# Kernel optimization log

Hardware: AMD Instinct MI355X
Metric: run time of the kernel (lower is better)

Reference implementation:

```python
import jax, jax.numpy as jnp
import numpy as np

SEQ_LEN = 768
PRED_LEN = 192
ENC_IN = 321
BATCH = 2
N_ORDER = 256
MULTISCALE = (1, 2, 4)
MODES = 32  # min(32, min(pred_len, seq_len)//2)


def _transition(N):
    Q = np.arange(N, dtype=np.float64)
    R = (2 * Q + 1)[:, None]
    j, i = np.meshgrid(Q, Q)
    A = np.where(i < j, -1, (-1.0) ** (i - j + 1)) * R
    B = (-1.0) ** Q[:, None] * R
    return A, B


def _hippo_legt(N, dt):
    # bilinear (Tustin) discretization, identical to scipy.signal.cont2discrete(..., method='bilinear')
    A, Bc = _transition(N)
    I = np.eye(N)
    M = I - (dt / 2.0) * A
    Ad = np.linalg.solve(M, I + (dt / 2.0) * A)
    Bd = np.linalg.solve(M, dt * Bc)[:, 0]
    # eval_matrix: Legendre P_n(1 - 2*vals), vals = arange(0, 1, dt)
    vals = np.arange(0.0, 1.0, dt)
    x = 1.0 - 2.0 * vals
    P = np.zeros((len(vals), N))
    P[:, 0] = 1.0
    if N > 1:
        P[:, 1] = x
    for n in range(1, N - 1):
        P[:, n + 1] = ((2 * n + 1) * x * P[:, n] - n * P[:, n - 1]) / (n + 1)
    return Ad.astype(np.float32), Bd.astype(np.float32), P.astype(np.float32)


def setup_inputs() -> dict:
    key = jax.random.key(0)
    k = jax.random.split(key, 6)
    A_l, B_l, E_l = [], [], []
    for ms in MULTISCALE:
        Ad, Bd, E = _hippo_legt(N_ORDER, 1.0 / PRED_LEN / ms)
        A_l.append(Ad); B_l.append(Bd); E_l.append(jnp.asarray(E))
    scale = 1.0 / (N_ORDER * N_ORDER)
    return {
        "history_data": jax.random.normal(k[0], (BATCH, SEQ_LEN, ENC_IN, 1), jnp.float32),
        "future_data": jax.random.normal(k[1], (BATCH, PRED_LEN, ENC_IN, 1), jnp.float32),
        "affine_weight": jnp.ones((1, 1, ENC_IN), jnp.float32),
        "affine_bias": jnp.zeros((1, 1, ENC_IN), jnp.float32),
        "A_stack": jnp.asarray(np.stack(A_l)),            # [3, N, N]
        "B_stack": jnp.asarray(np.stack(B_l)),            # [3, N]
        "E0": E_l[0], "E1": E_l[1], "E2": E_l[2],        # [ms*pred, N]
        "wr": scale * jax.random.uniform(k[2], (3, N_ORDER, N_ORDER, MODES), jnp.float32),
        "wi": scale * jax.random.uniform(k[3], (3, N_ORDER, N_ORDER, MODES), jnp.float32),
        "mlp_w": 0.3 * jax.random.normal(k[4], (1, 3), jnp.float32),
        "mlp_b": jnp.zeros((1,), jnp.float32),
        "batch_seen": 0, "epoch": 1, "train": 1,
    }


def _hippo_scan(x_in, A, Bv):
    # x_in: [B, Lw, H] -> states [Lw, B, H, N]
    inp = jnp.transpose(x_in, (1, 0, 2))  # [Lw, B, H]
    c0 = jnp.zeros(x_in.shape[:1] + x_in.shape[2:] + (A.shape[0],), x_in.dtype)  # [B, H, N]
    def step(c, f):
        c = c @ A.T + f[..., None] * Bv
        return c, c
    _, cs = jax.lax.scan(step, c0, inp)
    return cs


def _forward(history_data, affine_weight, affine_bias, A_stack, B_stack, evals, wr, wi, mlp_w, mlp_b):
    x_enc = history_data[:, :, :, 0]                      # [B, L, H]
    means = jax.lax.stop_gradient(jnp.mean(x_enc, axis=1, keepdims=True))
    x = x_enc - means
    stdev = jax.lax.stop_gradient(jnp.sqrt(jnp.mean(x * x, axis=1, keepdims=True) + 1e-5))
    x = x / stdev * affine_weight + affine_bias

    x_decs = []
    for i, ms in enumerate(MULTISCALE):
        Lw = ms * PRED_LEN
        x_in = x[:, -Lw:]                                  # [B, Lw, H]
        cs = _hippo_scan(x_in, A_stack[i], B_stack[i])     # [Lw, B, H, N]
        xc = jnp.transpose(cs, (1, 2, 3, 0))               # [B, H, N, Lw]
        # spectral conv: rfft -> complex mode mixing over N -> irfft
        xf = jnp.fft.rfft(xc)                              # [B, H, N, Lw//2+1]
        a = xf[..., :MODES]
        W = wr[i] + 1j * wi[i]                             # [N, N, MODES]
        of = jnp.einsum('bjix,iox->bjox', a, W)
        out_ft = jnp.pad(of, ((0, 0), (0, 0), (0, 0), (0, Lw // 2 + 1 - MODES)))
        o = jnp.fft.irfft(out_ft, n=Lw)                    # [B, H, N, Lw]
        x_dec_c = o[:, :, :, PRED_LEN - 1]                 # [B, H, N]
        x_dec = x_dec_c @ evals[i][-PRED_LEN:].T           # [B, H, pred]
        x_decs.append(x_dec)

    xd = jnp.stack(x_decs, axis=-1)                        # [B, H, pred, 3]
    xd = jnp.einsum('bhpk,k->bhp', xd, mlp_w[0]) + mlp_b[0]
    xd = jnp.transpose(xd, (0, 2, 1))                      # [B, pred, H]
    xd = (xd - affine_bias) / (affine_weight + 1e-10)
    xd = xd * stdev + means
    return xd[..., None]                                   # [B, pred, H, 1]


def reference(history_data, future_data, affine_weight, affine_bias, A_stack, B_stack, E0, E1, E2, wr, wi, mlp_w, mlp_b, batch_seen, epoch, train):
    return _forward(history_data, affine_weight, affine_bias, A_stack, B_stack, (E0, E1, E2), wr, wi, mlp_w, mlp_b)
```

## Files before the change

### kernel.cpp

```cpp
#include <hip/hip_runtime.h>

#define SEQ 768
#define PRED 192
#define ENC 321
#define NB 2
#define BE (NB*ENC)
#define CH 32

typedef float vf2 __attribute__((ext_vector_type(2)));
typedef short s4v __attribute__((ext_vector_type(4)));
typedef short s8v __attribute__((ext_vector_type(8)));
typedef float f32x4 __attribute__((ext_vector_type(4)));

union F4V2 { float4 f4; vf2 v2[2]; };
union S8U { s4v h[2]; s8v v; };

__device__ __forceinline__ float4 ldg4(const float* p) {
    return *reinterpret_cast<const float4*>(p);
}
__device__ __forceinline__ s8v ldg8s(const unsigned short* p) {
    return *reinterpret_cast<const s8v*>(p);
}
__device__ __forceinline__ void pklo(vf2& c, vf2 a, vf2 b) {
    asm("v_pk_fma_f32 %0, %1, %2, %0 op_sel:[0,0,0] op_sel_hi:[0,1,1]"
        : "+v"(c) : "v"(a), "v"(b));
}
__device__ __forceinline__ void pkhi(vf2& c, vf2 a, vf2 b) {
    asm("v_pk_fma_f32 %0, %1, %2, %0 op_sel:[1,0,0] op_sel_hi:[1,1,1]"
        : "+v"(c) : "v"(a), "v"(b));
}

__device__ __forceinline__ unsigned short f2bf(float f) {
    unsigned int u = __float_as_uint(f);
    u = (u + 0x7fffu + ((u >> 16) & 1u)) >> 16;
    return (unsigned short)u;
}
__device__ __forceinline__ float bf2f(unsigned short h) {
    return __uint_as_float(((unsigned int)h) << 16);
}

__host__ __device__ __forceinline__ int d_Lw(int s)    { return s==0?192:(s==1?384:768); }
__host__ __device__ __forceinline__ int d_Hoff(int s)  { return s==0?0:(s==1?49152:147456); }
__host__ __device__ __forceinline__ int d_twoff(int s) { return s==0?0:(s==1?6144:18432); }
__host__ __device__ __forceinline__ int d_Coff(int s)  { return s==0?0:(s==1?3145728:9437184); }
__host__ __device__ __forceinline__ int d_rowoff(int s){ return s==0?0:(s==1?192:576); }

__global__ void __launch_bounds__(256) k_init0(
    float2* __restrict__ twm, float2* __restrict__ gtm,
    const float* __restrict__ Ast, const float* __restrict__ Bst,
    float* __restrict__ apow, float* __restrict__ Hbuf,
    const float* __restrict__ hist, float* __restrict__ ps, float* __restrict__ ps2,
    const float* __restrict__ wr, const float* __restrict__ wi,
    unsigned short* __restrict__ Bph, unsigned short* __restrict__ Bpl)
{
    __shared__ float smem[128*36];
    int bid = blockIdx.x;
    int t = threadIdx.x;
    if (bid < 168) {
        int i = bid*256 + t;
        if (i >= 43008) return;
        int s, rem;
        if (i < 6144)       { s=0; rem=i; }
        else if (i < 18432) { s=1; rem=i-6144; }
        else                { s=2; rem=i-18432; }
        int Lw = d_Lw(s);
        int k = rem & 31, m = rem >> 5;
        const float TWO_PI = 6.28318530717958647692f;
        int km = (k*m) % Lw;
        float c, sn;
        sincosf(TWO_PI * km / Lw, &sn, &c);
        twm[i] = make_float2(c, -sn);
        int e = (k*(PRED-1-m)) % Lw; if (e < 0) e += Lw;
        float c2, s2v;
        sincosf(TWO_PI * e / Lw, &s2v, &c2);
        float coef = (k==0 ? 1.f : 2.f) / (float)Lw;
        gtm[i] = make_float2(coef*c2, coef*s2v);
    } else if (bid < 936) {
        int i = (bid-168)*256 + t;
        if (i < 3*65536) apow[i] = Ast[i];
        if (i < 3*256) {
            int s = i >> 8, n = i & 255;
            Hbuf[d_Hoff(s) + n] = Bst[i];
        }
    } else if (bid < 1032) {
        int r = bid - 936;
        int bx = r % 6, b = (r/6) % 2, z = r / 12;
        int jx = t & 63, ty = t >> 6;
        int j = bx*64 + jx;
        float s = 0.f, s2 = 0.f;
        if (j < ENC) {
            int t0 = z*96;
            for (int tt = t0 + ty; tt < t0 + 96; tt += 4) {
                float v = hist[(size_t)b*SEQ*ENC + (size_t)tt*ENC + j];
                s += v; s2 += v*v;
            }
        }
        float* l1 = smem;
        float* l2 = smem + 256;
        l1[ty*64+jx] = s; l2[ty*64+jx] = s2;
        __syncthreads();
        if (ty == 0 && j < ENC) {
            float S  = l1[jx]+l1[64+jx]+l1[128+jx]+l1[192+jx];
            float S2 = l2[jx]+l2[64+jx]+l2[128+jx]+l2[192+jx];
            ps [((size_t)z*2 + b)*ENC + j] = S;
            ps2[((size_t)z*2 + b)*ENC + j] = S2;
        }
    } else {
        int r = bid - 1032;
        int o  = r & 255;
        int q0 = ((r >> 8) & 1) * 128;
        int s  = r >> 9;
        const float* wrS = wr + (size_t)s*2097152;
        const float* wiS = wi + (size_t)s*2097152;
        unsigned short* BphS = Bph + (size_t)s*4194304;
        unsigned short* BplS = Bpl + (size_t)s*4194304;
        float (*ldsq)[36] = reinterpret_cast<float(*)[36]>(smem);
        int qr = t >> 1, half = (t & 1)*16;
        int kk = t & 31, qc = t >> 5;
        for (int c = 0; c < 2; c++) {
            const float* W = (c ? wiS : wrS) + (size_t)(q0+qr)*8192 + o*32 + half;
            float4 v0 = ldg4(W), v1 = ldg4(W+4), v2 = ldg4(W+8), v3 = ldg4(W+12);
            __syncthreads();
            *reinterpret_cast<float4*>(&ldsq[qr][half+0])  = v0;
            *reinterpret_cast<float4*>(&ldsq[qr][half+4])  = v1;
            *reinterpret_cast<float4*>(&ldsq[qr][half+8])  = v2;
            *reinterpret_cast<float4*>(&ldsq[qr][half+12]) = v3;
            __syncthreads();
            unsigned short hbuf[16], lbuf[16];
            #pragma unroll
            for (int j = 0; j < 16; j++) {
                float f = ldsq[qc*16 + j][kk];
                unsigned short h = f2bf(f);
                hbuf[j] = h;
                lbuf[j] = f2bf(f - bf2f(h));
            }
            int col = o*64 + kk*2 + c;
            int qb  = q0 + qc*16;
            size_t off = (size_t)(qb >> 5)*524288 + (size_t)col*32 + (qb & 31);
            #pragma unroll
            for (int j = 0; j < 2; j++) {
                *reinterpret_cast<s8v*>(BphS + off + j*8) = *reinterpret_cast<s8v*>(&hbuf[j*8]);
                *reinterpret_cast<s8v*>(BplS + off + j*8) = *reinterpret_cast<s8v*>(&lbuf[j*8]);
            }
        }
    }
}

__global__ void k_stats2(const float* __restrict__ ps, const float* __restrict__ ps2,
                         float* __restrict__ meanb, float* __restrict__ stdb) {
    int i = blockIdx.x*256 + threadIdx.x;
    if (i >= BE) return;
    int b = i / ENC, j = i - b*ENC;
    float S = 0.f, S2 = 0.f;
    #pragma unroll
    for (int z = 0; z < 8; z++) {
        S  += ps [((size_t)z*2 + b)*ENC + j];
        S2 += ps2[((size_t)z*2 + b)*ENC + j];
    }
    float m   = S * (1.f/SEQ);
    float var = S2 * (1.f/SEQ) - m*m;
    meanb[b*ENC+j] = m;
    stdb[b*ENC+j]  = sqrtf(var + 1e-5f);
}

__global__ void k_norm(const float* __restrict__ hist,
                       const float* __restrict__ meanb, const float* __restrict__ stdb,
                       const float* __restrict__ aw, const float* __restrict__ ab,
                       float* __restrict__ xn) {
    int i = blockIdx.x*256 + threadIdx.x;
    if (i >= NB*SEQ*ENC) return;
    int j = i % ENC;
    int b = i / (SEQ*ENC);
    float v = (hist[i] - meanb[b*ENC+j]) / stdb[b*ENC+j];
    xn[i] = v * aw[j] + ab[j];
}

__device__ __forceinline__ void gemm32nt(float* As, float* Bs,
    const float* __restrict__ A, int Arows, const float* __restrict__ B,
    float* __restrict__ C, int m0, int n0)
{
    int tid = threadIdx.x;
    int tm = tid >> 4, tn = tid & 15;
    int lr = tid >> 3, lq = (tid & 7)*4;
    float a00=0.f,a01=0.f,a10=0.f,a11=0.f;
    for (int kt = 0; kt < 256; kt += 32) {
        __syncthreads();
        float4 fa = ldg4(A + (size_t)(m0+lr)*256 + kt + lq);
        float4 fb = ldg4(B + (size_t)(n0+lr)*256 + kt + lq);
        As[lr*33+lq]=fa.x; As[lr*33+lq+1]=fa.y; As[lr*33+lq+2]=fa.z; As[lr*33+lq+3]=fa.w;
        Bs[lr*33+lq]=fb.x; Bs[lr*33+lq+1]=fb.y; Bs[lr*33+lq+2]=fb.z; Bs[lr*33+lq+3]=fb.w;
        __syncthreads();
        #pragma unroll
        for (int q = 0; q < 32; q++) {
            float x0 = As[(tm*2)*33+q],  x1 = As[(tm*2+1)*33+q];
            float y0 = Bs[(tn*2)*33+q],  y1 = Bs[(tn*2+1)*33+q];
            a00 = fmaf(x0,y0,a00); a01 = fmaf(x0,y1,a01);
            a10 = fmaf(x1,y0,a10); a11 = fmaf(x1,y1,a11);
        }
    }
    int m = m0 + tm*2, n = n0 + tn*2;
    if (m < Arows)   { C[(size_t)m*256+n]     = a00; C[(size_t)m*256+n+1]     = a01; }
    if (m+1 < Arows) { C[(size_t)(m+1)*256+n] = a10; C[(size_t)(m+1)*256+n+1] = a11; }
}

__device__ __forceinline__ void gemm32nn(float* As, float* Bs,
    const float* __restrict__ A, const float* __restrict__ B,
    float* __restrict__ C, int m0, int n0)
{
    int tid = threadIdx.x;
    int tm = tid >> 4, tn = tid & 15;
    int lr = tid >> 3, lq = (tid & 7)*4;
    float a00=0.f,a01=0.f,a10=0.f,a11=0.f;
    for (int kt = 0; kt < 256; kt += 32) {
        __syncthreads();
        float4 fa = ldg4(A + (size_t)(m0+lr)*256 + kt + lq);
        float4 fb = ldg4(B + (size_t)(kt+lr)*256 + n0 + lq);
        As[lr*33+lq]=fa.x; As[lr*33+lq+1]=fa.y; As[lr*33+lq+2]=fa.z; As[lr*33+lq+3]=fa.w;
        Bs[lr*33+lq]=fb.x; Bs[lr*33+lq+1]=fb.y; Bs[lr*33+lq+2]=fb.z; Bs[lr*33+lq+3]=fb.w;
        __syncthreads();
        #pragma unroll
        for (int q = 0; q < 32; q++) {
            float x0 = As[(tm*2)*33+q], x1 = As[(tm*2+1)*33+q];
            float y0 = Bs[q*33+tn*2],   y1 = Bs[q*33+tn*2+1];
            a00 = fmaf(x0,y0,a00); a01 = fmaf(x0,y1,a01);
            a10 = fmaf(x1,y0,a10); a11 = fmaf(x1,y1,a11);
        }
    }
    int m = m0 + tm*2, n = n0 + tn*2;
    C[(size_t)m*256+n]     = a00; C[(size_t)m*256+n+1]     = a01;
    C[(size_t)(m+1)*256+n] = a10; C[(size_t)(m+1)*256+n+1] = a11;
}

__global__ void __launch_bounds__(256) k_hlevel32(float* __restrict__ Hbuf,
                                                  float* __restrict__ apow,
                                                  int par, int mc) {
    __shared__ float As[32*33];
    __shared__ float Bs[32*33];
    int s = blockIdx.z;
    int Lw = d_Lw(s);
    const float* Asrc = apow + (size_t)par*196608 + (size_t)s*65536;
    float* Adst       = apow + (size_t)(1-par)*196608 + (size_t)s*65536;
    float* H = Hbuf + d_Hoff(s);
    int yt = blockIdx.y, xt = blockIdx.x;
    if (yt < 8) {
        if (mc >= Lw) return;
        int rows = min(mc, Lw - mc);
        if (yt*32 >= rows) return;
        gemm32nt(As, Bs, H, rows, Asrc, H + (size_t)mc*256, yt*32, xt*32);
    } else {
        if (2*mc >= Lw) return;
        gemm32nn(As, Bs, Asrc, Asrc, Adst, (yt-8)*32, xt*32);
    }
}

__global__ void k_split_h(const float* __restrict__ Hbuf,
                          unsigned short* __restrict__ Hh,
                          unsigned short* __restrict__ Hl) {
    int i = blockIdx.x*256 + threadIdx.x;
    if (i >= 344064) return;
    int s, rem;
    if (i < 49152)       { s=0; rem=i; }
    else if (i < 147456) { s=1; rem=i-49152; }
    else                 { s=2; rem=i-147456; }
    int Lw = d_Lw(s);
    int row = rem >> 8, q = rem & 255;
    float f = Hbuf[i];
    unsigned short h = f2bf(f);
    float l = f - bf2f(h);
    size_t off = (size_t)d_Hoff(s) + (size_t)(q >> 5)*((size_t)Lw*32) + (size_t)row*32 + (q & 31);
    Hh[off] = h;
    Hl[off] = f2bf(l);
}

__device__ __forceinline__ s8v lds_frag(const short* s, int idx) {
    S8U u;
    u.h[0] = *reinterpret_cast<const s4v*>(s + idx);
    u.h[1] = *reinterpret_cast<const s4v*>(s + idx + 4);
    return u.v;
}

__global__ void __launch_bounds__(256) k_cgemm_mfma(
    const unsigned short* __restrict__ Hh, const unsigned short* __restrict__ Hl,
    const unsigned short* __restrict__ Bph, const unsigned short* __restrict__ Bpl,
    float* __restrict__ C)
{
    int t = threadIdx.x;
    int nwg = gridDim.x;
    int cpx = nwg >> 3;
    int bid = blockIdx.x;
    int lid = (bid & 7)*cpx + (bid >> 3);
    int s, local, mt;
    if (lid < 256)      { s = 0; local = lid;       mt = 2; }
    else if (lid < 640) { s = 1; local = lid - 256; mt = 3; }
    else                { s = 2; local = lid - 640; mt = 6; }
    int Lw = d_Lw(s);
    int bx = local % mt, by = local / mt;
    int m0 = bx*128, n0 = by*128;

    const unsigned short* HhS = Hh + d_Hoff(s);
    const unsigned short* HlS = Hl + d_Hoff(s);
    const unsigned short* BphS = Bph + (size_t)s*4194304;
    const unsigned short* BplS = Bpl + (size_t)s*4194304;
    float* CS = C + d_Coff(s);

    __shared__ short sA[2][128*36];
    __shared__ short sB[2][128*36];
    int lane = t & 63, wave = t >> 6;
    int wm = wave >> 1, wn = wave & 1;
    int srow = t >> 1, shalf = (t & 1)*16;
    size_t strideA = (size_t)Lw*32;
    size_t aRow = (size_t)(m0 + srow)*32 + shalf;
    size_t bRow = (size_t)(n0 + srow)*32 + shalf;
    int sOff = srow*36 + shalf;

    f32x4 acc[4][4];
    #pragma unroll
    for (int i = 0; i < 4; i++)
        #pragma unroll
        for (int j = 0; j < 4; j++)
            acc[i][j] = (f32x4){0.f, 0.f, 0.f, 0.f};

    S8U ah0, ah1, al0, al1, bh0, bh1, bl0, bl1;
    ah0.v = ldg8s(HhS + aRow);
    ah1.v = ldg8s(HhS + aRow + 8);
    al0.v = ldg8s(HlS + aRow);
    al1.v = ldg8s(HlS + aRow + 8);
    bh0.v = ldg8s(BphS + bRow);
    bh1.v = ldg8s(BphS + bRow + 8);
    bl0.v = ldg8s(BplS + bRow);
    bl1.v = ldg8s(BplS + bRow + 8);

    for (int kt = 0; kt < 256; kt += 32) {
        __syncthreads();
        *reinterpret_cast<s4v*>(&sA[0][sOff+0])  = ah0.h[0];
        *reinterpret_cast<s4v*>(&sA[0][sOff+4])  = ah0.h[1];
        *reinterpret_cast<s4v*>(&sA[0][sOff+8])  = ah1.h[0];
        *reinterpret_cast<s4v*>(&sA[0][sOff+12]) = ah1.h[1];
        *reinterpret_cast<s4v*>(&sA[1][sOff+0])  = al0.h[0];
        *reinterpret_cast<s4v*>(&sA[1][sOff+4])  = al0.h[1];
        *reinterpret_cast<s4v*>(&sA[1][sOff+8])  = al1.h[0];
        *reinterpret_cast<s4v*>(&sA[1][sOff+12]) = al1.h[1];
        *reinterpret_cast<s4v*>(&sB[0][sOff+0])  = bh0.h[0];
        *reinterpret_cast<s4v*>(&sB[0][sOff+4])  = bh0.h[1];
        *reinterpret_cast<s4v*>(&sB[0][sOff+8])  = bh1.h[0];
        *reinterpret_cast<s4v*>(&sB[0][sOff+12]) = bh1.h[1];
        *reinterpret_cast<s4v*>(&sB[1][sOff+0])  = bl0.h[0];
        *reinterpret_cast<s4v*>(&sB[1][sOff+4])  = bl0.h[1];
        *reinterpret_cast<s4v*>(&sB[1][sOff+8])  = bl1.h[0];
        *reinterpret_cast<s4v*>(&sB[1][sOff+12]) = bl1.h[1];
        __syncthreads();
        if (kt + 32 < 256) {
            int kb = (kt >> 5) + 1;
            ah0.v = ldg8s(HhS + kb*strideA + aRow);
            ah1.v = ldg8s(HhS + kb*strideA + aRow + 8);
            al0.v = ldg8s(HlS + kb*strideA + aRow);
            al1.v = ldg8s(HlS + kb*strideA + aRow + 8);
            bh0.v = ldg8s(BphS + (size_t)kb*524288 + bRow);
            bh1.v = ldg8s(BphS + (size_t)kb*524288 + bRow + 8);
            bl0.v = ldg8s(BplS + (size_t)kb*524288 + bRow);
            bl1.v = ldg8s(BplS + (size_t)kb*524288 + bRow + 8);
        }
        int klane = (lane >> 4) << 3;
        s8v Bfh[4], Bfl[4];
        #pragma unroll
        for (int tn = 0; tn < 4; tn++) {
            int cb = (wn*64 + tn*16 + (lane & 15))*36 + klane;
            Bfh[tn] = lds_frag(sB[0], cb);
            Bfl[tn] = lds_frag(sB[1], cb);
        }
        #pragma unroll
        for (int tm = 0; tm < 4; tm++) {
            int ca = (wm*64 + tm*16 + (lane & 15))*36 + klane;
            s8v Ah = lds_frag(sA[0], ca);
            s8v Al = lds_frag(sA[1], ca);
            #pragma unroll
            for (int tn = 0; tn < 4; tn++) {
                acc[tm][tn] = __builtin_amdgcn_mfma_f32_16x16x32_bf16(Ah, Bfh[tn], acc[tm][tn], 0, 0, 0);
                acc[tm][tn] = __builtin_amdgcn_mfma_f32_16x16x32_bf16(Ah, Bfl[tn], acc[tm][tn], 0, 0, 0);
                acc[tm][tn] = __builtin_amdgcn_mfma_f32_16x16x32_bf16(Al, Bfh[tn], acc[tm][tn], 0, 0, 0);
            }
        }
    }
    int r0 = (lane >> 4)*4, cc = lane & 15;
    #pragma unroll
    for (int tm = 0; tm < 4; tm++) {
        #pragma unroll
        for (int tn = 0; tn < 4; tn++) {
            int gcol = n0 + wn*64 + tn*16 + cc;
            int og = gcol >> 6, rem = gcol & 63;
            float* cp = CS + (size_t)og*((size_t)Lw*64) + rem;
            #pragma unroll
            for (int reg = 0; reg < 4; reg++) {
                int r = m0 + wm*64 + tm*16 + r0 + reg;
                if (r < Lw) cp[(size_t)r*64] = acc[tm][tn][reg];
            }
        }
    }
}

__global__ void k_cscan1(const float2* __restrict__ Call2, const float2* __restrict__ twm,
                         float2* __restrict__ psum) {
    int cg = blockIdx.x;
    int s  = (cg < 6) ? 0 : (cg < 18) ? 1 : 2;
    int cl = cg - ((s==0)?0:(s==1)?6:18);
    int Lw = d_Lw(s);
    int tid = threadIdx.x;
    int k = tid & 31, ol = tid >> 5;
    int o = blockIdx.y*8 + ol;
    const float2* tws = twm + d_twoff(s);
    const float2* Co = Call2 + (d_Coff(s) >> 1) + (size_t)o*((size_t)Lw*32);
    int mbase = cl*CH;
    float pr = 0.f, pi = 0.f;
    for (int mm = 0; mm < CH; mm++) {
        int m = mbase + mm;
        float2 cc = Co[(size_t)m*32 + k];
        float2 t  = tws[(size_t)m*32 + k];
        pr = fmaf(t.x, cc.x, pr); pr = fmaf(-t.y, cc.y, pr);
        pi = fmaf(t.x, cc.y, pi); pi = fmaf(t.y, cc.x, pi);
    }
    psum[((size_t)cg)*8192 + o*32 + k] = make_float2(pr, pi);
}

__global__ void k_cscan2(const float2* __restrict__ Call2, const float2* __restrict__ twm,
                         const float2* __restrict__ gtm, const float2* __restrict__ psum,
                         float* __restrict__ Qall) {
    int cg = blockIdx.x;
    int s  = (cg < 6) ? 0 : (cg < 18) ? 1 : 2;
    int cgbase = (s==0)?0:(s==1)?6:18;
    int cl = cg - cgbase;
    int Lw = d_Lw(s);
    float* Qrow = Qall + (size_t)d_rowoff(s)*256;
    int tid = threadIdx.x;
    int k = tid & 31, ol = tid >> 5;
    int o = blockIdx.y*8 + ol;
    const float2* tws = twm + d_twoff(s);
    const float2* gts = gtm + d_twoff(s);
    const float2* Co = Call2 + (d_Coff(s) >> 1) + (size_t)o*((size_t)Lw*32);
    float pr = 0.f, pi = 0.f;
    for (int c = 0; c < cl; c++) {
        float2 p = psum[((size_t)(cgbase+c))*8192 + o*32 + k];
        pr += p.x; pi += p.y;
    }
    int mbase = cl*CH;
    for (int mm = 0; mm < CH; mm++) {
        int m = mbase + mm;
        float2 cc = Co[(size_t)m*32 + k];
        float2 t  = tws[(size_t)m*32 + k];
        pr = fmaf(t.x, cc.x, pr); pr = fmaf(-t.y, cc.y, pr);
        pi = fmaf(t.x, cc.y, pi); pi = fmaf(t.y, cc.x, pi);
        int r = Lw - 1 - m;
        float2 g = gts[(size_t)r*32 + k];
        float qv = g.x*pr - g.y*pi;
        qv += __shfl_xor(qv, 16);
        qv += __shfl_xor(qv, 8);
        qv += __shfl_xor(qv, 4);
        qv += __shfl_xor(qv, 2);
        qv += __shfl_xor(qv, 1);
        if (k == 0) Qrow[(size_t)r*256 + o] = qv;
    }
}

__device__ __forceinline__ void gemm64nt(
    const float* __restrict__ A, int lda, int Arows,
    const float* __restrict__ B, int ldb,
    float* __restrict__ C, int ldc, int m0, int n0, int K)
{
    __shared__ __align__(16) float AsT[16][68];
    __shared__ __align__(16) float BsT[16][68];
    int tid = threadIdx.x;
    int tm = tid >> 4, tn = tid & 15;
    int lr = tid >> 2, lq = (tid & 3)*4;
    bool aok = (m0 + lr) < Arows;
    const float* Ap = A + (size_t)(m0+lr)*lda + lq;
    const float* Bp = B + (size_t)(n0+lr)*ldb + lq;
    float4 fa = aok ? ldg4(Ap) : make_float4(0.f,0.f,0.f,0.f);
    float4 fb = ldg4(Bp);
    vf2 acc[4][2] = {};
    for (int kt = 0; kt < K; kt += 16) {
        __syncthreads();
        AsT[lq+0][lr]=fa.x; AsT[lq+1][lr]=fa.y; AsT[lq+2][lr]=fa.z; AsT[lq+3][lr]=fa.w;
        BsT[lq+0][lr]=fb.x; BsT[lq+1][lr]=fb.y; BsT[lq+2][lr]=fb.z; BsT[lq+3][lr]=fb.w;
        __syncthreads();
        if (kt + 16 < K) {
            fa = aok ? ldg4(Ap + kt + 16) : make_float4(0.f,0.f,0.f,0.f);
            fb = ldg4(Bp + kt + 16);
        }
        #pragma unroll
        for (int q = 0; q < 16; q++) {
            F4V2 ua, ub;
            ua.f4 = *reinterpret_cast<float4*>(&AsT[q][tm*4]);
            ub.f4 = *reinterpret_cast<float4*>(&BsT[q][tn*4]);
            #pragma unroll
            for (int ra = 0; ra < 2; ra++)
                #pragma unroll
                for (int cp = 0; cp < 2; cp++) {
                    pklo(acc[2*ra+0][cp], ua.v2[ra], ub.v2[cp]);
                    pkhi(acc[2*ra+1][cp], ua.v2[ra], ub.v2[cp]);
                }
        }
    }
    #pragma unroll
    for (int r = 0; r < 4; r++) {
        int m = m0 + tm*4 + r; if (m >= Arows) continue;
        float4 o4 = make_float4(acc[r][0].x, acc[r][0].y, acc[r][1].x, acc[r][1].y);
        *reinterpret_cast<float4*>(C + (size_t)m*ldc + n0 + tn*4) = o4;
    }
}

__global__ void __launch_bounds__(256) k_tgemm(const float* __restrict__ Qall,
                                               const float* __restrict__ E0,
                                               const float* __restrict__ E1,
                                               const float* __restrict__ E2,
                                               float* __restrict__ T) {
    int mtg = blockIdx.x;
    int s, lm, Lw, rowoff, Toff;
    if (mtg < 3)      { s=0; lm=mtg;   Lw=192; rowoff=0;   Toff=0; }
    else if (mtg < 9) { s=1; lm=mtg-3; Lw=384; rowoff=192; Toff=36864; }
    else              { s=2; lm=mtg-9; Lw=768; rowoff=576; Toff=110592; }
    const float* Es = (s==0) ? E0 : ((s==1) ? E1 : E2);
    gemm64nt(Qall + (size_t)rowoff*256, 256, Lw,
             Es + (size_t)(Lw-192)*256, 256,
             T + Toff, 192, lm*64, blockIdx.y*64, 256);
}

__global__ void k_mtot(const float* __restrict__ T, const float* __restrict__ mlpw,
                       float* __restrict__ M) {
    int i = blockIdx.x*256 + threadIdx.x;
    if (i >= 192*768) return;
    int p = i / 768, t = i % 768;
    float v = mlpw[2] * T[110592 + (size_t)t*192 + p];
    if (t >= 384) v += mlpw[1] * T[36864 + (size_t)(t-384)*192 + p];
    if (t >= 576) v += mlpw[0] * T[(size_t)(t-576)*192 + p];
    M[i] = v;
}

__global__ void __launch_bounds__(256) k_finalA(
    const float* __restrict__ M, const float* __restrict__ xn,
    float* __restrict__ partial)
{
    __shared__ float Ms[4*128];
    int tid = threadIdx.x;
    int pg = blockIdx.y, z = blockIdx.z;
    #pragma unroll
    for (int e = tid; e < 512; e += 256) {
        int u = e >> 7, tt = e & 127;
        Ms[e] = M[(size_t)(pg*4 + u)*768 + z*128 + tt];
    }
    __syncthreads();
    int cc = blockIdx.x*256 + tid;
    if (cc >= BE) return;
    int b = (cc >= ENC) ? 1 : 0;
    int j = cc - b*ENC;
    const float* xp = xn + (size_t)b*SEQ*ENC + (size_t)(z*128)*ENC + j;
    float a0 = 0.f, a1 = 0.f, a2 = 0.f, a3 = 0.f;
    #pragma unroll 8
    for (int t = 0; t < 128; t++) {
        float xv = xp[(size_t)t*ENC];
        a0 = fmaf(Ms[t],       xv, a0);
        a1 = fmaf(Ms[128 + t], xv, a1);
        a2 = fmaf(Ms[256 + t], xv, a2);
        a3 = fmaf(Ms[384 + t], xv, a3);
    }
    size_t base = ((size_t)z*192 + pg*4)*BE + cc;
    partial[base]        = a0;
    partial[base + BE]   = a1;
    partial[base + 2*BE] = a2;
    partial[base + 3*BE] = a3;
}

__global__ void __launch_bounds__(256) k_finalB(
    const float* __restrict__ partial,
    const float* __restrict__ aw, const float* __restrict__ ab,
    const float* __restrict__ meanb, const float* __restrict__ stdb,
    const float* __restrict__ mlpb, float* __restrict__ out)
{
    int i = blockIdx.x*256 + threadIdx.x;
    if (i >= 192*BE) return;
    int p = i / BE, cc = i - p*BE;
    float s = 0.f;
    #pragma unroll
    for (int z = 0; z < 6; z++)
        s += partial[((size_t)z*192 + p)*BE + cc];
    int b = (cc >= ENC) ? 1 : 0;
    int j = cc - b*ENC;
    float v = (s + mlpb[0] - ab[j]) / (aw[j] + 1e-10f);
    v = v * stdb[b*ENC+j] + meanb[b*ENC+j];
    out[(size_t)b*(PRED*ENC) + (size_t)p*ENC + j] = v;
}

extern "C" void kernel_launch(void* const* d_in, const int* in_sizes, int n_in,
                              void* d_out, int out_size, void* d_ws, size_t ws_size,
                              hipStream_t stream)
{
    const float* hist = (const float*)d_in[0];
    const float* aw   = (const float*)d_in[2];
    const float* ab   = (const float*)d_in[3];
    const float* Ast  = (const float*)d_in[4];
    const float* Bst  = (const float*)d_in[5];
    const float* E0   = (const float*)d_in[6];
    const float* E1   = (const float*)d_in[7];
    const float* E2   = (const float*)d_in[8];
    const float* wr   = (const float*)d_in[9];
    const float* wi   = (const float*)d_in[10];
    const float* mlpw = (const float*)d_in[11];
    const float* mlpb = (const float*)d_in[12];
    float* out = (float*)d_out;

    float* w = (float*)d_ws;
    float* xn    = w; w += 493056;
    float* meanb = w; w += 642;
    float* stdb  = w; w += 642;
    float* pstat = w; w += 5136;
    float* pstat2= w; w += 5136;
    float* Hbuf  = w; w += 344064;
    float* apow  = w; w += 393216;
    float2* twm  = (float2*)w; w += 86016;
    float2* gtm  = (float2*)w; w += 86016;
    float2* psum = (float2*)w; w += 688128;
    unsigned short* Hh  = (unsigned short*)w; w += 172032;
    unsigned short* Hl  = (unsigned short*)w; w += 172032;
    unsigned short* Bph = (unsigned short*)w; w += 6291456;
    unsigned short* Bpl = (unsigned short*)w; w += 6291456;
    float* Call  = w; w += 22020096;
    float* Qall  = w; w += 344064;
    float* Tbuf  = w; w += 258048;
    float* Mt    = w; w += 147456;
    float* fpart = w; w += 739584;

    k_init0<<<2568, 256, 0, stream>>>(twm, gtm, Ast, Bst, apow, Hbuf,
                                      hist, pstat, pstat2, wr, wi, Bph, Bpl);
    k_stats2<<<3, 256, 0, stream>>>(pstat, pstat2, meanb, stdb);
    k_norm<<<1926, 256, 0, stream>>>(hist, meanb, stdb, aw, ab, xn);
    for (int lev = 0; lev < 10; lev++)
        k_hlevel32<<<dim3(8,16,3), 256, 0, stream>>>(Hbuf, apow, lev & 1, 1 << lev);
    k_split_h<<<1344, 256, 0, stream>>>(Hbuf, Hh, Hl);

    k_cgemm_mfma<<<1408, 256, 0, stream>>>(Hh, Hl, Bph, Bpl, Call);
    k_cscan1<<<dim3(42, 32), 256, 0, stream>>>((const float2*)Call, twm, psum);
    k_cscan2<<<dim3(42, 32), 256, 0, stream>>>((const float2*)Call, twm, gtm, psum, Qall);

    k_tgemm<<<dim3(21,3), 256, 0, stream>>>(Qall, E0, E1, E2, Tbuf);
    k_mtot<<<576, 256, 0, stream>>>(Tbuf, mlpw, Mt);
    k_finalA<<<dim3(3, 48, 6), 256, 0, stream>>>(Mt, xn, fpart);
    k_finalB<<<482, 256, 0, stream>>>(fpart, aw, ab, meanb, stdb, mlpb, out);
}
```

Baseline: 266.6 us.

## Fuse stats, bf16 split and mixing-weight kernels into neighbouring kernels

Removes three small kernel launches. The mean/std finalisation moves into the normalisation kernel, which now redoes the 8-way partial-sum reduction in every thread. The bf16 hi/lo split of H is done in the epilogue of the doubling-scan GEMM and in init for the first row. The M = sum of weighted T matrices is computed directly while loading shared memory in finalA. This saves launch overhead and intermediate buffer traffic, at the cost of redundant reduction work and scattered 16-bit stores in the GEMM epilogue.

```diff
diff --git a/kernel.cpp b/kernel.cpp
--- a/kernel.cpp
+++ b/kernel.cpp
@@ -49,6 +49,7 @@
     float2* __restrict__ twm, float2* __restrict__ gtm,
     const float* __restrict__ Ast, const float* __restrict__ Bst,
     float* __restrict__ apow, float* __restrict__ Hbuf,
+    unsigned short* __restrict__ Hh, unsigned short* __restrict__ Hl,
     const float* __restrict__ hist, float* __restrict__ ps, float* __restrict__ ps2,
     const float* __restrict__ wr, const float* __restrict__ wi,
     unsigned short* __restrict__ Bph, unsigned short* __restrict__ Bpl)
@@ -80,7 +81,13 @@
         if (i < 3*65536) apow[i] = Ast[i];
         if (i < 3*256) {
             int s = i >> 8, n = i & 255;
-            Hbuf[d_Hoff(s) + n] = Bst[i];
+            int Lw = d_Lw(s);
+            float v = Bst[i];
+            Hbuf[d_Hoff(s) + n] = v;
+            size_t off = (size_t)d_Hoff(s) + (size_t)(n >> 5)*((size_t)Lw*32) + (n & 31);
+            unsigned short h = f2bf(v);
+            Hh[off] = h;
+            Hl[off] = f2bf(v - bf2f(h));
         }
     } else if (bid < 1032) {
         int r = bid - 936;
@@ -146,11 +153,17 @@
     }
 }
 
-__global__ void k_stats2(const float* __restrict__ ps, const float* __restrict__ ps2,
-                         float* __restrict__ meanb, float* __restrict__ stdb) {
+__global__ void k_norm(const float* __restrict__ hist,
+                       const float* __restrict__ ps, const float* __restrict__ ps2,
+                       const float* __restrict__ aw, const float* __restrict__ ab,
+                       float* __restrict__ xn,
+                       float* __restrict__ meanb, float* __restrict__ stdb) {
     int i = blockIdx.x*256 + threadIdx.x;
-    if (i >= BE) return;
-    int b = i / ENC, j = i - b*ENC;
+    if (i >= NB*SEQ*ENC) return;
+    int j = i % ENC;
+    int bt = i / ENC;
+    int b = i / (SEQ*ENC);
+    int t = bt - b*SEQ;
     float S = 0.f, S2 = 0.f;
     #pragma unroll
     for (int z = 0; z < 8; z++) {
@@ -159,25 +172,17 @@
     }
     float m   = S * (1.f/SEQ);
     float var = S2 * (1.f/SEQ) - m*m;
-    meanb[b*ENC+j] = m;
-    stdb[b*ENC+j]  = sqrtf(var + 1e-5f);
-}
-
-__global__ void k_norm(const float* __restrict__ hist,
-                       const float* __restrict__ meanb, const float* __restrict__ stdb,
-                       const float* __restrict__ aw, const float* __restrict__ ab,
-                       float* __restrict__ xn) {
-    int i = blockIdx.x*256 + threadIdx.x;
-    if (i >= NB*SEQ*ENC) return;
-    int j = i % ENC;
-    int b = i / (SEQ*ENC);
-    float v = (hist[i] - meanb[b*ENC+j]) / stdb[b*ENC+j];
+    float sd  = sqrtf(var + 1e-5f);
+    if (t == 0) { meanb[b*ENC+j] = m; stdb[b*ENC+j] = sd; }
+    float v = (hist[i] - m) / sd;
     xn[i] = v * aw[j] + ab[j];
 }
 
-__device__ __forceinline__ void gemm32nt(float* As, float* Bs,
+__device__ __forceinline__ void gemm32nt_split(float* As, float* Bs,
     const float* __restrict__ A, int Arows, const float* __restrict__ B,
-    float* __restrict__ C, int m0, int n0)
+    float* __restrict__ C, int m0, int n0,
+    unsigned short* __restrict__ Hh, unsigned short* __restrict__ Hl,
+    size_t hoff, int Lw, int mc)
 {
     int tid = threadIdx.x;
     int tm = tid >> 4, tn = tid & 15;
@@ -199,8 +204,16 @@
         }
     }
     int m = m0 + tm*2, n = n0 + tn*2;
-    if (m < Arows)   { C[(size_t)m*256+n]     = a00; C[(size_t)m*256+n+1]     = a01; }
-    if (m+1 < Arows) { C[(size_t)(m+1)*256+n] = a10; C[(size_t)(m+1)*256+n+1] = a11; }
+    #define WR1(mm, nn, vv) { \
+        C[(size_t)(mm)*256+(nn)] = (vv); \
+        int grow = mc + (mm); \
+        size_t off = hoff + (size_t)((nn) >> 5)*((size_t)Lw*32) + (size_t)grow*32 + ((nn) & 31); \
+        unsigned short hh = f2bf(vv); \
+        Hh[off] = hh; \
+        Hl[off] = f2bf((vv) - bf2f(hh)); }
+    if (m < Arows)   { WR1(m,   n, a00); WR1(m,   n+1, a01); }
+    if (m+1 < Arows) { WR1(m+1, n, a10); WR1(m+1, n+1, a11); }
+    #undef WR1
 }
 
 __device__ __forceinline__ void gemm32nn(float* As, float* Bs,
@@ -233,6 +246,8 @@
 
 __global__ void __launch_bounds__(256) k_hlevel32(float* __restrict__ Hbuf,
                                                   float* __restrict__ apow,
+                                                  unsigned short* __restrict__ Hh,
+                                                  unsigned short* __restrict__ Hl,
                                                   int par, int mc) {
     __shared__ float As[32*33];
     __shared__ float Bs[32*33];
@@ -246,30 +261,12 @@
         if (mc >= Lw) return;
         int rows = min(mc, Lw - mc);
         if (yt*32 >= rows) return;
-        gemm32nt(As, Bs, H, rows, Asrc, H + (size_t)mc*256, yt*32, xt*32);
+        gemm32nt_split(As, Bs, H, rows, Asrc, H + (size_t)mc*256, yt*32, xt*32,
+                       Hh, Hl, (size_t)d_Hoff(s), Lw, mc);
     } else {
         if (2*mc >= Lw) return;
         gemm32nn(As, Bs, Asrc, Asrc, Adst, (yt-8)*32, xt*32);
     }
-}
-
-__global__ void k_split_h(const float* __restrict__ Hbuf,
-                          unsigned short* __restrict__ Hh,
-                          unsigned short* __restrict__ Hl) {
-    int i = blockIdx.x*256 + threadIdx.x;
-    if (i >= 344064) return;
-    int s, rem;
-    if (i < 49152)       { s=0; rem=i; }
-    else if (i < 147456) { s=1; rem=i-49152; }
-    else                 { s=2; rem=i-147456; }
-    int Lw = d_Lw(s);
-    int row = rem >> 8, q = rem & 255;
-    float f = Hbuf[i];
-    unsigned short h = f2bf(f);
-    float l = f - bf2f(h);
-    size_t off = (size_t)d_Hoff(s) + (size_t)(q >> 5)*((size_t)Lw*32) + (size_t)row*32 + (q & 31);
-    Hh[off] = h;
-    Hl[off] = f2bf(l);
 }
 
 __device__ __forceinline__ s8v lds_frag(const short* s, int idx) {
@@ -523,28 +520,22 @@
              T + Toff, 192, lm*64, blockIdx.y*64, 256);
 }
 
-__global__ void k_mtot(const float* __restrict__ T, const float* __restrict__ mlpw,
-                       float* __restrict__ M) {
-    int i = blockIdx.x*256 + threadIdx.x;
-    if (i >= 192*768) return;
-    int p = i / 768, t = i % 768;
-    float v = mlpw[2] * T[110592 + (size_t)t*192 + p];
-    if (t >= 384) v += mlpw[1] * T[36864 + (size_t)(t-384)*192 + p];
-    if (t >= 576) v += mlpw[0] * T[(size_t)(t-576)*192 + p];
-    M[i] = v;
-}
-
 __global__ void __launch_bounds__(256) k_finalA(
-    const float* __restrict__ M, const float* __restrict__ xn,
-    float* __restrict__ partial)
+    const float* __restrict__ T, const float* __restrict__ mlpw,
+    const float* __restrict__ xn, float* __restrict__ partial)
 {
     __shared__ float Ms[4*128];
     int tid = threadIdx.x;
     int pg = blockIdx.y, z = blockIdx.z;
+    float mw0 = mlpw[0], mw1 = mlpw[1], mw2 = mlpw[2];
     #pragma unroll
     for (int e = tid; e < 512; e += 256) {
         int u = e >> 7, tt = e & 127;
-        Ms[e] = M[(size_t)(pg*4 + u)*768 + z*128 + tt];
+        int p = pg*4 + u, t = z*128 + tt;
+        float v = mw2 * T[110592 + (size_t)t*192 + p];
+        if (t >= 384) v += mw1 * T[36864 + (size_t)(t-384)*192 + p];
+        if (t >= 576) v += mw0 * T[(size_t)(t-576)*192 + p];
+        Ms[e] = v;
     }
     __syncthreads();
     int cc = blockIdx.x*256 + tid;
@@ -624,23 +615,19 @@
     float* Call  = w; w += 22020096;
     float* Qall  = w; w += 344064;
     float* Tbuf  = w; w += 258048;
-    float* Mt    = w; w += 147456;
     float* fpart = w; w += 739584;
 
-    k_init0<<<2568, 256, 0, stream>>>(twm, gtm, Ast, Bst, apow, Hbuf,
+    k_init0<<<2568, 256, 0, stream>>>(twm, gtm, Ast, Bst, apow, Hbuf, Hh, Hl,
                                       hist, pstat, pstat2, wr, wi, Bph, Bpl);
-    k_stats2<<<3, 256, 0, stream>>>(pstat, pstat2, meanb, stdb);
-    k_norm<<<1926, 256, 0, stream>>>(hist, meanb, stdb, aw, ab, xn);
+    k_norm<<<1926, 256, 0, stream>>>(hist, pstat, pstat2, aw, ab, xn, meanb, stdb);
     for (int lev = 0; lev < 10; lev++)
-        k_hlevel32<<<dim3(8,16,3), 256, 0, stream>>>(Hbuf, apow, lev & 1, 1 << lev);
-    k_split_h<<<1344, 256, 0, stream>>>(Hbuf, Hh, Hl);
+        k_hlevel32<<<dim3(8,16,3), 256, 0, stream>>>(Hbuf, apow, Hh, Hl, lev & 1, 1 << lev);
 
     k_cgemm_mfma<<<1408, 256, 0, stream>>>(Hh, Hl, Bph, Bpl, Call);
     k_cscan1<<<dim3(42, 32), 256, 0, stream>>>((const float2*)Call, twm, psum);
     k_cscan2<<<dim3(42, 32), 256, 0, stream>>>((const float2*)Call, twm, gtm, psum, Qall);
 
     k_tgemm<<<dim3(21,3), 256, 0, stream>>>(Qall, E0, E1, E2, Tbuf);
-    k_mtot<<<576, 256, 0, stream>>>(Tbuf, mlpw, Mt);
-    k_finalA<<<dim3(3, 48, 6), 256, 0, stream>>>(Mt, xn, fpart);
+    k_finalA<<<dim3(3, 48, 6), 256, 0, stream>>>(Tbuf, mlpw, xn, fpart);
     k_finalB<<<482, 256, 0, stream>>>(fpart, aw, ab, meanb, stdb, mlpb, out);
 }
```

After: 263.1 us (median of 3 runs). No clear change (-1.3%).
